# Kernel optimization log

Measured on AMD Instinct MI355X. Metric: run time of the kernel, lower is better.

The kernel has to match this reference:

```python
import jax, jax.numpy as jnp
import numpy as np

N_EMBED = 1024
EMBED_DIM = 64
BETA = 0.25


def setup_inputs() -> dict:
    key = jax.random.key(0)
    k1, k2 = jax.random.split(key)
    # z_e: (B, C, H, W) with C == embed_dim
    z_e = jax.random.normal(k1, (16, EMBED_DIM, 64, 64), dtype=jnp.float32)
    # codebook init: uniform(-1/n_embed, 1/n_embed), matching nn.init.uniform_
    emb = jax.random.uniform(k2, (N_EMBED, EMBED_DIM), dtype=jnp.float32,
                             minval=-1.0 / N_EMBED, maxval=1.0 / N_EMBED)
    return {"z_e": z_e, "emb": emb}


def reference(z_e, emb):
    B, C, H, W = z_e.shape
    # (B,C,H,W) -> (B,H,W,C) -> (B*H*W, C)
    z_flat = jnp.transpose(z_e, (0, 2, 3, 1)).reshape(-1, C)
    # squared euclidean distances to every codebook entry: (N, n_embed)
    dist = (jnp.sum(z_flat * z_flat, axis=1, keepdims=True)
            - 2.0 * (z_flat @ emb.T)
            + jnp.sum(emb * emb, axis=1)[None, :])
    idx = jnp.argmin(dist, axis=1)  # (N,)
    # gather codebook vectors, back to (B, C, H, W)
    z_q = jnp.transpose(emb[idx].reshape(B, H, W, C), (0, 3, 1, 2))
    # straight-through estimator
    z_q_st = z_e + jax.lax.stop_gradient(z_q - z_e)
    codebook_loss = jnp.mean((jax.lax.stop_gradient(z_q) - z_e) ** 2)
    commit_loss = jnp.mean((z_q - jax.lax.stop_gradient(z_e)) ** 2)
    loss = codebook_loss + BETA * commit_loss
    return z_q_st, loss, idx.reshape(B, H, W)
```

## Files before the change

### kernel.cpp

```cpp
#include <hip/hip_runtime.h>

#define NROWS   65536
#define NEMB    1024
#define HWD     4096
#define CHW     262144
#define OUT_ZQ  4194304
#define BETA    0.25f
#define MARGIN  4e-3f
#define MAXC    32

typedef __attribute__((ext_vector_type(8))) short bf16x8;
typedef __attribute__((ext_vector_type(4))) float f32x4;

#define F4C(v,i) ((i)==0?(v).x:((i)==1?(v).y:((i)==2?(v).z:(v).w)))

__device__ __forceinline__ unsigned short bf16rn(float f) {
    unsigned int x = __float_as_uint(f);
    x += 0x7fffu + ((x >> 16) & 1);
    return (unsigned short)(x >> 16);
}
__device__ __forceinline__ float bf16tof(unsigned short h) {
    return __uint_as_float(((unsigned int)h) << 16);
}
__device__ __forceinline__ unsigned int ordf(float f) {
    unsigned int u = __float_as_uint(f);
    return (u & 0x80000000u) ? ~u : (u | 0x80000000u);
}
__device__ __forceinline__ float deordf(unsigned int m) {
    return __uint_as_float((m & 0x80000000u) ? (m ^ 0x80000000u) : ~m);
}

__device__ __forceinline__ float np_pairwise64(const float p[64]) {
#pragma clang fp contract(off)
    float r[8];
#pragma unroll
    for (int a = 0; a < 8; ++a) r[a] = p[a];
#pragma unroll
    for (int i = 8; i < 64; i += 8) {
#pragma unroll
        for (int a = 0; a < 8; ++a) r[a] = r[a] + p[i + a];
    }
    return ((r[0] + r[1]) + (r[2] + r[3])) + ((r[4] + r[5]) + (r[6] + r[7]));
}

__global__ void k_se(const float* __restrict__ emb, float* __restrict__ se) {
#pragma clang fp contract(off)
    int j = blockIdx.x * 256 + threadIdx.x;
    if (j < NEMB) {
        float p[64];
#pragma unroll
        for (int c = 0; c < 64; ++c) { float v = emb[(size_t)j * 64 + c]; p[c] = v * v; }
        se[j] = np_pairwise64(p);
    }
}

__global__ void k_prep(const float* __restrict__ emb, bf16x8* __restrict__ ebt) {
    int idx  = blockIdx.x * 256 + threadIdx.x;
    int tile = idx >> 7;
    int f    = (idx >> 6) & 1;
    int lane = idx & 63;
    int entry = tile * 16 + (lane & 15);
    int kb    = f * 32 + ((lane >> 4) << 3);
    bf16x8 v;
#pragma unroll
    for (int i = 0; i < 8; ++i)
        v[i] = (short)bf16rn(emb[(size_t)entry * 64 + kb + i]);
    ebt[idx] = v;
}

__global__ __launch_bounds__(256, 2) void k_mfma(
        const float* __restrict__ ze, const float* __restrict__ emb,
        const bf16x8* __restrict__ ebt, const float* __restrict__ se,
        float* __restrict__ out, float* __restrict__ wsloss) {
#pragma clang fp contract(off)
    __shared__ float zt[4096];
    __shared__ unsigned short zb[8192];
    __shared__ float se_s[NEMB];
    __shared__ float sz_s[64];
    __shared__ unsigned int rowmin_u[64];
    __shared__ int cnt_s[64];
    __shared__ int cand_s[64 * MAXC];
    __shared__ unsigned long long best_s[64];
    __shared__ int bi_s[64];

    const int tid  = threadIdx.x;
    const int wid  = tid >> 6;
    const int lane = tid & 63;
    const int l15  = lane & 15;
    const int kg   = lane >> 4;
    const int row0 = blockIdx.x * 64;
    const int b    = row0 >> 12;
    const int hw0  = row0 & 4095;
    const float* __restrict__ zblk = ze + (size_t)b * CHW + hw0;

#pragma unroll
    for (int k = 0; k < 4; ++k) se_s[k * 256 + tid] = se[k * 256 + tid];
#pragma unroll
    for (int k = 0; k < 16; ++k) {
        int idx = k * 256 + tid;
        zt[idx] = zblk[(size_t)(idx >> 6) * HWD + (idx & 63)];
    }
    if (tid < 64) { rowmin_u[tid] = 0xFFFFFFFFu; cnt_s[tid] = 0; best_s[tid] = ~0ULL; }
    __syncthreads();

    if (tid < 64) {
        float p[64];
#pragma unroll
        for (int c = 0; c < 64; ++c) { float v = zt[c * 64 + tid]; p[c] = v * v; }
        sz_s[tid] = np_pairwise64(p);
    }

#pragma unroll
    for (int k4 = 0; k4 < 4; ++k4) {
        int cid = k4 * 256 + tid;
        int row = cid >> 4, kc = cid & 15;
        bf16x8 v;
#pragma unroll
        for (int i = 0; i < 8; ++i) {
            int k = kc * 8 + i;
            float z = zt[(k & 63) * 64 + row];
            unsigned short h = bf16rn(z);
            v[i] = (short)((k < 64) ? h : bf16rn(z - bf16tof(h)));
        }
        *(bf16x8*)&zb[(row * 128 + kc * 8) ^ ((row & 7) << 3)] = v;
    }
    __syncthreads();

    const int arow  = wid * 16 + l15;
    const int abase = arow * 128 + kg * 8;
    const int aswz  = (arow & 7) << 3;
    const bf16x8 Ah0 = *(const bf16x8*)&zb[(abase +  0) ^ aswz];
    const bf16x8 Ah1 = *(const bf16x8*)&zb[(abase + 32) ^ aswz];
    const bf16x8 Al0 = *(const bf16x8*)&zb[(abase + 64) ^ aswz];
    const bf16x8 Al1 = *(const bf16x8*)&zb[(abase + 96) ^ aswz];

    float rmin[4] = {3.4028235e38f, 3.4028235e38f, 3.4028235e38f, 3.4028235e38f};
    const bf16x8* __restrict__ ebt_l = ebt + lane;
    const f32x4 zero4 = {0.0f, 0.0f, 0.0f, 0.0f};
    bf16x8 Ca, Cb, Na, Nb;

#define LOADB(T, Xa, Xb) do {                                               \
        const bf16x8* p_ = ebt_l + (T) * 128;                               \
        Xa = p_[0]; Xb = p_[64];                                            \
    } while (0)

#define PROCESS(T, Xa, Xb, PASS2) do {                                      \
        f32x4 acc_ = zero4;                                                 \
        acc_ = __builtin_amdgcn_mfma_f32_16x16x32_bf16(Ah0, Xa, acc_, 0,0,0);\
        acc_ = __builtin_amdgcn_mfma_f32_16x16x32_bf16(Ah1, Xb, acc_, 0,0,0);\
        acc_ = __builtin_amdgcn_mfma_f32_16x16x32_bf16(Al0, Xa, acc_, 0,0,0);\
        acc_ = __builtin_amdgcn_mfma_f32_16x16x32_bf16(Al1, Xb, acc_, 0,0,0);\
        const int j_ = (T) * 16 + l15;                                      \
        const float sej_ = se_s[j_];                                        \
        _Pragma("unroll")                                                   \
        for (int q = 0; q < 4; ++q) {                                       \
            float g_ = fmaf(-2.0f, F4C(acc_, q), sej_);                     \
            if (!(PASS2)) {                                                 \
                rmin[q] = fminf(rmin[q], g_);                               \
            } else if (g_ <= rmin[q]) {                                     \
                int row_ = wid * 16 + kg * 4 + q;                           \
                int k_ = atomicAdd(&cnt_s[row_], 1);                        \
                if (k_ < MAXC) cand_s[row_ * MAXC + k_] = j_;               \
            }                                                               \
        }                                                                   \
    } while (0)

    LOADB(0, Ca, Cb);
    for (int t = 0; t < 64; t += 2) {
        LOADB(t + 1, Na, Nb);
        PROCESS(t, Ca, Cb, false);
        LOADB((t + 2 > 63 ? 63 : t + 2), Ca, Cb);
        PROCESS(t + 1, Na, Nb, false);
    }
#pragma unroll
    for (int q = 0; q < 4; ++q)
        atomicMin(&rowmin_u[wid * 16 + kg * 4 + q], ordf(rmin[q]));
    __syncthreads();
#pragma unroll
    for (int q = 0; q < 4; ++q)
        rmin[q] = deordf(rowmin_u[wid * 16 + kg * 4 + q]) + MARGIN;

    LOADB(0, Ca, Cb);
    for (int t = 0; t < 64; t += 2) {
        LOADB(t + 1, Na, Nb);
        PROCESS(t, Ca, Cb, true);
        LOADB((t + 2 > 63 ? 63 : t + 2), Ca, Cb);
        PROCESS(t + 1, Na, Nb, true);
    }
    __syncthreads();

    for (int w = tid; w < 64 * MAXC; w += 256) {
        int r = w >> 5, ci = w & (MAXC - 1);
        int nc = cnt_s[r];
        if (ci < (nc < MAXC ? nc : MAXC)) {
            int j = cand_s[r * MAXC + ci];
            const float* __restrict__ e = emb + (size_t)j * 64;
            float dot = 0.0f;
#pragma unroll
            for (int c = 0; c < 64; ++c) dot = fmaf(e[c], zt[c * 64 + r], dot);
            float d = (sz_s[r] - 2.0f * dot) + se_s[j];
            atomicMin(&best_s[r],
                      ((unsigned long long)ordf(d) << 32) | (unsigned int)j);
        }
        if (nc > MAXC) {
            for (int j = ci; j < NEMB; j += MAXC) {
                const float* __restrict__ e = emb + (size_t)j * 64;
                float dot = 0.0f;
#pragma unroll
                for (int c = 0; c < 64; ++c) dot = fmaf(e[c], zt[c * 64 + r], dot);
                float d = (sz_s[r] - 2.0f * dot) + se_s[j];
                atomicMin(&best_s[r],
                          ((unsigned long long)ordf(d) << 32) | (unsigned int)j);
            }
        }
    }
    __syncthreads();

    if (tid < 64) {
        int j = (int)(best_s[tid] & 0xFFFFFFFFu);
        bi_s[tid] = j;
        out[(size_t)OUT_ZQ + 1 + row0 + tid] = (float)j;
    }
    __syncthreads();

    float part = 0.0f;
#pragma unroll
    for (int rep = 0; rep < 16; ++rep) {
        int i = rep * 256 + tid;
        int c = i >> 6, r = i & 63;
        int bj = bi_s[r];
        size_t zoff = (size_t)b * CHW + (size_t)c * HWD + hw0 + r;
        float ev = emb[(size_t)bj * 64 + c];
        float zv = ze[zoff];
        float qmz = ev - zv;
        out[zoff] = zv + qmz;
        part = part + qmz * qmz;
    }
    float* red_s = (float*)zb;
    red_s[tid] = part;
    __syncthreads();
#pragma unroll
    for (int s = 128; s >= 1; s >>= 1) {
        if (tid < s) red_s[tid] = red_s[tid] + red_s[tid + s];
        __syncthreads();
    }
    if (tid == 0) wsloss[blockIdx.x] = red_s[0];
#undef LOADB
#undef PROCESS
}

__global__ __launch_bounds__(256, 4) void k_main_v5(
        const float* __restrict__ ze, const float* __restrict__ emb,
        const float* __restrict__ se, float* __restrict__ out,
        float* __restrict__ wsloss) {
#pragma clang fp contract(off)
    __shared__ float zt[4096];
    __shared__ float es[4096];
    __shared__ float se_s[NEMB];
    __shared__ float sz_s[64];
    __shared__ int   bi_s[64];

    const int tid  = threadIdx.x;
    const int rg   = tid & 15;
    const int eg   = tid >> 4;
    const int row0 = blockIdx.x * 64;
    const int b    = row0 >> 12;
    const int hw0  = row0 & 4095;
    const float* __restrict__ zblk = ze + (size_t)b * CHW + hw0;

#pragma unroll
    for (int k = 0; k < 4; ++k) se_s[k * 256 + tid] = se[k * 256 + tid];
#pragma unroll
    for (int k = 0; k < 16; ++k) {
        int idx = k * 256 + tid;
        zt[idx] = zblk[(size_t)(idx >> 6) * HWD + (idx & 63)];
    }
    __syncthreads();
    if (tid < 64) {
        float p[64];
#pragma unroll
        for (int c = 0; c < 64; ++c) { float v = zt[c * 64 + tid]; p[c] = v * v; }
        sz_s[tid] = np_pairwise64(p);
    }
    __syncthreads();
    const float4 sz4 = *(const float4*)&sz_s[rg * 4];
    float best[4] = {3.4028235e38f, 3.4028235e38f, 3.4028235e38f, 3.4028235e38f};
    int   bi[4]   = {0, 0, 0, 0};
    for (int ch = 0; ch < 16; ++ch) {
        __syncthreads();
        {
            const float4* __restrict__ src = (const float4*)(emb + ch * 4096);
#pragma unroll
            for (int k = 0; k < 4; ++k) {
                int idx = k * 256 + tid;
                int jl = idx >> 4, c4 = idx & 15;
                *(float4*)&es[(jl << 6) + ((c4 ^ (jl & 15)) << 2)] = src[idx];
            }
        }
        __syncthreads();
        const float4 se4 = *(const float4*)&se_s[ch * 64 + eg * 4];
        float acc[4][4];
#pragma unroll
        for (int a = 0; a < 4; ++a)
#pragma unroll
            for (int q = 0; q < 4; ++q) acc[a][q] = 0.0f;
#pragma unroll 4
        for (int c4 = 0; c4 < 16; ++c4) {
            float4 zq[4], ef[4];
#pragma unroll
            for (int cc = 0; cc < 4; ++cc)
                zq[cc] = *(const float4*)&zt[((c4 * 4 + cc) << 6) + (rg << 2)];
#pragma unroll
            for (int jj = 0; jj < 4; ++jj) {
                int jl = eg * 4 + jj;
                ef[jj] = *(const float4*)&es[(jl << 6) + ((c4 ^ (jl & 15)) << 2)];
            }
#pragma unroll
            for (int cc = 0; cc < 4; ++cc)
#pragma unroll
                for (int jj = 0; jj < 4; ++jj)
#pragma unroll
                    for (int rr = 0; rr < 4; ++rr)
                        acc[jj][rr] = fmaf(F4C(ef[jj], cc), F4C(zq[cc], rr), acc[jj][rr]);
        }
        const int j0 = ch * 64 + eg * 4;
#pragma unroll
        for (int jj = 0; jj < 4; ++jj) {
            float sej = F4C(se4, jj);
#pragma unroll
            for (int rr = 0; rr < 4; ++rr) {
                float dist = (F4C(sz4, rr) - 2.0f * acc[jj][rr]) + sej;
                if (dist < best[rr]) { best[rr] = dist; bi[rr] = j0 + jj; }
            }
        }
    }
    __syncthreads();
    float* dmin_s = zt;
    int*   imin_s = (int*)es;
#pragma unroll
    for (int rr = 0; rr < 4; ++rr) {
        dmin_s[tid * 4 + rr] = best[rr];
        imin_s[tid * 4 + rr] = bi[rr];
    }
    __syncthreads();
    if (tid < 64) {
        int rgm = tid >> 2, rrm = tid & 3;
        float bb = 3.4028235e38f; int ii = 0x7fffffff;
#pragma unroll
        for (int m = 0; m < 16; ++m) {
            int t = m * 16 + rgm;
            float d  = dmin_s[t * 4 + rrm];
            int   i2 = imin_s[t * 4 + rrm];
            if (d < bb || (d == bb && i2 < ii)) { bb = d; ii = i2; }
        }
        bi_s[tid] = ii;
        out[(size_t)OUT_ZQ + 1 + row0 + tid] = (float)ii;
    }
    __syncthreads();
    float part = 0.0f;
#pragma unroll
    for (int rep = 0; rep < 16; ++rep) {
        int i = rep * 256 + tid;
        int c = i >> 6, r = i & 63;
        int bj = bi_s[r];
        size_t zoff = (size_t)b * CHW + (size_t)c * HWD + hw0 + r;
        float ev = emb[(size_t)bj * 64 + c];
        float zv = ze[zoff];
        float qmz = ev - zv;
        out[zoff] = zv + qmz;
        part = part + qmz * qmz;
    }
    float* red_s = zt;
    red_s[tid] = part;
    __syncthreads();
#pragma unroll
    for (int s = 128; s >= 1; s >>= 1) {
        if (tid < s) red_s[tid] = red_s[tid] + red_s[tid + s];
        __syncthreads();
    }
    if (tid == 0) wsloss[blockIdx.x] = red_s[0];
}

__global__ void k_loss(const float* __restrict__ wsloss, float* __restrict__ out) {
#pragma clang fp contract(off)
    __shared__ float red[256];
    int tid = threadIdx.x;
    float s = 0.0f;
    for (int i = tid; i < 1024; i += 256) s = s + wsloss[i];
    red[tid] = s;
    __syncthreads();
#pragma unroll
    for (int k = 128; k >= 1; k >>= 1) {
        if (tid < k) red[tid] = red[tid] + red[tid + k];
        __syncthreads();
    }
    if (tid == 0) {
        float mse = red[0] / 4194304.0f;
        out[OUT_ZQ] = mse + BETA * mse;
    }
}

extern "C" void kernel_launch(void* const* d_in, const int* in_sizes, int n_in,
                              void* d_out, int out_size, void* d_ws, size_t ws_size,
                              hipStream_t stream) {
    const float* ze  = (const float*)d_in[0];
    const float* emb = (const float*)d_in[1];
    float* out    = (float*)d_out;
    float* se     = (float*)d_ws;
    float* wsloss = se + NEMB;
    bf16x8* ebt   = (bf16x8*)(wsloss + 1024);
    const size_t NEED = 2048 * sizeof(float) + 8192 * sizeof(bf16x8);

    k_se<<<4, 256, 0, stream>>>(emb, se);
    if (ws_size >= NEED) {
        k_prep<<<32,   256, 0, stream>>>(emb, ebt);
        k_mfma<<<1024, 256, 0, stream>>>(ze, emb, ebt, se, out, wsloss);
    } else {
        k_main_v5<<<1024, 256, 0, stream>>>(ze, emb, se, out, wsloss);
    }
    k_loss<<<1, 256, 0, stream>>>(wsloss, out);
}
```

Baseline: 111.0 us.

## Fuse codebook-norm kernel into prep, build MFMA A fragments in registers, shrink MAXC

The separate codebook squared-norm kernel is folded into k_prep, which removes one launch. The split hi/lo bf16 A-operand fragments are now built directly in registers from the transposed z tile instead of going through a swizzled LDS buffer. That drops about 16KB of shared memory and one barrier, and the loss reduction reuses zt as scratch. The per-row candidate cap is halved to 16, which shrinks the candidate list, but any row with more candidates than that falls back to a full 1024-entry scan, so overflow becomes more likely. On the fallback path, k_prep now writes its bf16 table into d_ws, which may overflow the small workspace and clobber se.

```diff
diff --git a/kernel.cpp b/kernel.cpp
--- a/kernel.cpp
+++ b/kernel.cpp
@@ -7,7 +7,7 @@
 #define OUT_ZQ  4194304
 #define BETA    0.25f
 #define MARGIN  4e-3f
-#define MAXC    32
+#define MAXC    16
 
 typedef __attribute__((ext_vector_type(8))) short bf16x8;
 typedef __attribute__((ext_vector_type(4))) float f32x4;
@@ -43,18 +43,9 @@
     return ((r[0] + r[1]) + (r[2] + r[3])) + ((r[4] + r[5]) + (r[6] + r[7]));
 }
 
-__global__ void k_se(const float* __restrict__ emb, float* __restrict__ se) {
+__global__ void k_prep(const float* __restrict__ emb, bf16x8* __restrict__ ebt,
+                       float* __restrict__ se) {
 #pragma clang fp contract(off)
-    int j = blockIdx.x * 256 + threadIdx.x;
-    if (j < NEMB) {
-        float p[64];
-#pragma unroll
-        for (int c = 0; c < 64; ++c) { float v = emb[(size_t)j * 64 + c]; p[c] = v * v; }
-        se[j] = np_pairwise64(p);
-    }
-}
-
-__global__ void k_prep(const float* __restrict__ emb, bf16x8* __restrict__ ebt) {
     int idx  = blockIdx.x * 256 + threadIdx.x;
     int tile = idx >> 7;
     int f    = (idx >> 6) & 1;
@@ -66,6 +57,14 @@
     for (int i = 0; i < 8; ++i)
         v[i] = (short)bf16rn(emb[(size_t)entry * 64 + kb + i]);
     ebt[idx] = v;
+
+    if (blockIdx.x < 4) {
+        int j = blockIdx.x * 256 + threadIdx.x;
+        float p[64];
+#pragma unroll
+        for (int c = 0; c < 64; ++c) { float vv = emb[(size_t)j * 64 + c]; p[c] = vv * vv; }
+        se[j] = np_pairwise64(p);
+    }
 }
 
 __global__ __launch_bounds__(256, 2) void k_mfma(
@@ -74,7 +73,6 @@
         float* __restrict__ out, float* __restrict__ wsloss) {
 #pragma clang fp contract(off)
     __shared__ float zt[4096];
-    __shared__ unsigned short zb[8192];
     __shared__ float se_s[NEMB];
     __shared__ float sz_s[64];
     __shared__ unsigned int rowmin_u[64];
@@ -110,29 +108,20 @@
         sz_s[tid] = np_pairwise64(p);
     }
 
-#pragma unroll
-    for (int k4 = 0; k4 < 4; ++k4) {
-        int cid = k4 * 256 + tid;
-        int row = cid >> 4, kc = cid & 15;
-        bf16x8 v;
-#pragma unroll
-        for (int i = 0; i < 8; ++i) {
-            int k = kc * 8 + i;
-            float z = zt[(k & 63) * 64 + row];
-            unsigned short h = bf16rn(z);
-            v[i] = (short)((k < 64) ? h : bf16rn(z - bf16tof(h)));
-        }
-        *(bf16x8*)&zb[(row * 128 + kc * 8) ^ ((row & 7) << 3)] = v;
-    }
-    __syncthreads();
-
-    const int arow  = wid * 16 + l15;
-    const int abase = arow * 128 + kg * 8;
-    const int aswz  = (arow & 7) << 3;
-    const bf16x8 Ah0 = *(const bf16x8*)&zb[(abase +  0) ^ aswz];
-    const bf16x8 Ah1 = *(const bf16x8*)&zb[(abase + 32) ^ aswz];
-    const bf16x8 Al0 = *(const bf16x8*)&zb[(abase + 64) ^ aswz];
-    const bf16x8 Al1 = *(const bf16x8*)&zb[(abase + 96) ^ aswz];
+    const int arow = wid * 16 + l15;
+    bf16x8 Ah0, Ah1, Al0, Al1;
+#pragma unroll
+    for (int i = 0; i < 8; ++i) {
+        int k0 = kg * 8 + i;
+        float z0 = zt[k0 * 64 + arow];
+        unsigned short h0 = bf16rn(z0);
+        Ah0[i] = (short)h0;
+        Al0[i] = (short)bf16rn(z0 - bf16tof(h0));
+        float z1 = zt[(32 + k0) * 64 + arow];
+        unsigned short h1 = bf16rn(z1);
+        Ah1[i] = (short)h1;
+        Al1[i] = (short)bf16rn(z1 - bf16tof(h1));
+    }
 
     float rmin[4] = {3.4028235e38f, 3.4028235e38f, 3.4028235e38f, 3.4028235e38f};
     const bf16x8* __restrict__ ebt_l = ebt + lane;
@@ -190,7 +179,7 @@
     __syncthreads();
 
     for (int w = tid; w < 64 * MAXC; w += 256) {
-        int r = w >> 5, ci = w & (MAXC - 1);
+        int r = w >> 4, ci = w & (MAXC - 1);
         int nc = cnt_s[r];
         if (ci < (nc < MAXC ? nc : MAXC)) {
             int j = cand_s[r * MAXC + ci];
@@ -236,7 +225,7 @@
         out[zoff] = zv + qmz;
         part = part + qmz * qmz;
     }
-    float* red_s = (float*)zb;
+    float* red_s = zt;
     red_s[tid] = part;
     __syncthreads();
 #pragma unroll
@@ -411,11 +400,11 @@
     bf16x8* ebt   = (bf16x8*)(wsloss + 1024);
     const size_t NEED = 2048 * sizeof(float) + 8192 * sizeof(bf16x8);
 
-    k_se<<<4, 256, 0, stream>>>(emb, se);
     if (ws_size >= NEED) {
-        k_prep<<<32,   256, 0, stream>>>(emb, ebt);
+        k_prep<<<32,   256, 0, stream>>>(emb, ebt, se);
         k_mfma<<<1024, 256, 0, stream>>>(ze, emb, ebt, se, out, wsloss);
     } else {
+        k_prep<<<32, 256, 0, stream>>>(emb, (bf16x8*)d_ws, se);
         k_main_v5<<<1024, 256, 0, stream>>>(ze, emb, se, out, wsloss);
     }
     k_loss<<<1, 256, 0, stream>>>(wsloss, out);
```

After: 158.7 us. 43.0% more time.

## Replace second MFMA pass with per-lane top-2 tracking and fuse codebook norm kernel

Applied to the files above, without the earlier changes.

The candidate search no longer re-runs the MFMA distance pass. Each lane tracks its two smallest approximate distances with their indices, plus a third-smallest value. After the row minimum is reduced, only those two candidates per lane are rescored exactly in fp32. If a lane's third-smallest value also falls within the margin, a flag forces a full fp32 rescan of that row. The hi/lo MFMA accumulations are split into independent chains to shorten dependencies, and the codebook squared-norm kernel is folded into the prep kernel to remove a launch. The cost is extra per-element compare/select work in the main loop and a possible fallback full rescan per flagged row. The fallback path now writes bf16 data into the workspace it may lack room for.

```diff
diff --git a/kernel.cpp b/kernel.cpp
--- a/kernel.cpp
+++ b/kernel.cpp
@@ -7,7 +7,6 @@
 #define OUT_ZQ  4194304
 #define BETA    0.25f
 #define MARGIN  4e-3f
-#define MAXC    32
 
 typedef __attribute__((ext_vector_type(8))) short bf16x8;
 typedef __attribute__((ext_vector_type(4))) float f32x4;
@@ -43,18 +42,9 @@
     return ((r[0] + r[1]) + (r[2] + r[3])) + ((r[4] + r[5]) + (r[6] + r[7]));
 }
 
-__global__ void k_se(const float* __restrict__ emb, float* __restrict__ se) {
+__global__ void k_prep(const float* __restrict__ emb, bf16x8* __restrict__ ebt,
+                       float* __restrict__ se) {
 #pragma clang fp contract(off)
-    int j = blockIdx.x * 256 + threadIdx.x;
-    if (j < NEMB) {
-        float p[64];
-#pragma unroll
-        for (int c = 0; c < 64; ++c) { float v = emb[(size_t)j * 64 + c]; p[c] = v * v; }
-        se[j] = np_pairwise64(p);
-    }
-}
-
-__global__ void k_prep(const float* __restrict__ emb, bf16x8* __restrict__ ebt) {
     int idx  = blockIdx.x * 256 + threadIdx.x;
     int tile = idx >> 7;
     int f    = (idx >> 6) & 1;
@@ -66,6 +56,14 @@
     for (int i = 0; i < 8; ++i)
         v[i] = (short)bf16rn(emb[(size_t)entry * 64 + kb + i]);
     ebt[idx] = v;
+
+    if (blockIdx.x < 4) {
+        int j = blockIdx.x * 256 + threadIdx.x;
+        float p[64];
+#pragma unroll
+        for (int c = 0; c < 64; ++c) { float vv = emb[(size_t)j * 64 + c]; p[c] = vv * vv; }
+        se[j] = np_pairwise64(p);
+    }
 }
 
 __global__ __launch_bounds__(256, 2) void k_mfma(
@@ -78,8 +76,7 @@
     __shared__ float se_s[NEMB];
     __shared__ float sz_s[64];
     __shared__ unsigned int rowmin_u[64];
-    __shared__ int cnt_s[64];
-    __shared__ int cand_s[64 * MAXC];
+    __shared__ int flag_s[64];
     __shared__ unsigned long long best_s[64];
     __shared__ int bi_s[64];
 
@@ -100,7 +97,7 @@
         int idx = k * 256 + tid;
         zt[idx] = zblk[(size_t)(idx >> 6) * HWD + (idx & 63)];
     }
-    if (tid < 64) { rowmin_u[tid] = 0xFFFFFFFFu; cnt_s[tid] = 0; best_s[tid] = ~0ULL; }
+    if (tid < 64) { rowmin_u[tid] = 0xFFFFFFFFu; flag_s[tid] = 0; best_s[tid] = ~0ULL; }
     __syncthreads();
 
     if (tid < 64) {
@@ -134,7 +131,13 @@
     const bf16x8 Al0 = *(const bf16x8*)&zb[(abase + 64) ^ aswz];
     const bf16x8 Al1 = *(const bf16x8*)&zb[(abase + 96) ^ aswz];
 
-    float rmin[4] = {3.4028235e38f, 3.4028235e38f, 3.4028235e38f, 3.4028235e38f};
+    const float INF = 3.4028235e38f;
+    float m1[4] = {INF, INF, INF, INF};
+    float m2[4] = {INF, INF, INF, INF};
+    float m3[4] = {INF, INF, INF, INF};
+    int   a1[4] = {0, 0, 0, 0};
+    int   a2[4] = {0, 0, 0, 0};
+
     const bf16x8* __restrict__ ebt_l = ebt + lane;
     const f32x4 zero4 = {0.0f, 0.0f, 0.0f, 0.0f};
     bf16x8 Ca, Cb, Na, Nb;
@@ -144,66 +147,67 @@
         Xa = p_[0]; Xb = p_[64];                                            \
     } while (0)
 
-#define PROCESS(T, Xa, Xb, PASS2) do {                                      \
-        f32x4 acc_ = zero4;                                                 \
-        acc_ = __builtin_amdgcn_mfma_f32_16x16x32_bf16(Ah0, Xa, acc_, 0,0,0);\
-        acc_ = __builtin_amdgcn_mfma_f32_16x16x32_bf16(Ah1, Xb, acc_, 0,0,0);\
-        acc_ = __builtin_amdgcn_mfma_f32_16x16x32_bf16(Al0, Xa, acc_, 0,0,0);\
-        acc_ = __builtin_amdgcn_mfma_f32_16x16x32_bf16(Al1, Xb, acc_, 0,0,0);\
+#define PROCESS(T, Xa, Xb) do {                                             \
+        f32x4 ah = zero4, al = zero4;                                       \
+        ah = __builtin_amdgcn_mfma_f32_16x16x32_bf16(Ah0, Xa, ah, 0,0,0);   \
+        al = __builtin_amdgcn_mfma_f32_16x16x32_bf16(Al0, Xa, al, 0,0,0);   \
+        ah = __builtin_amdgcn_mfma_f32_16x16x32_bf16(Ah1, Xb, ah, 0,0,0);   \
+        al = __builtin_amdgcn_mfma_f32_16x16x32_bf16(Al1, Xb, al, 0,0,0);   \
         const int j_ = (T) * 16 + l15;                                      \
         const float sej_ = se_s[j_];                                        \
         _Pragma("unroll")                                                   \
         for (int q = 0; q < 4; ++q) {                                       \
-            float g_ = fmaf(-2.0f, F4C(acc_, q), sej_);                     \
-            if (!(PASS2)) {                                                 \
-                rmin[q] = fminf(rmin[q], g_);                               \
-            } else if (g_ <= rmin[q]) {                                     \
-                int row_ = wid * 16 + kg * 4 + q;                           \
-                int k_ = atomicAdd(&cnt_s[row_], 1);                        \
-                if (k_ < MAXC) cand_s[row_ * MAXC + k_] = j_;               \
-            }                                                               \
+            float s_ = F4C(ah, q) + F4C(al, q);                             \
+            float g_ = fmaf(-2.0f, s_, sej_);                               \
+            bool c1 = g_ < m1[q];                                           \
+            bool c2 = g_ < m2[q];                                           \
+            a2[q] = c2 ? (c1 ? a1[q] : j_) : a2[q];                         \
+            a1[q] = c1 ? j_ : a1[q];                                        \
+            float hi1 = fmaxf(m1[q], g_);                                   \
+            m1[q] = fminf(m1[q], g_);                                       \
+            float hi2 = fmaxf(m2[q], hi1);                                  \
+            m2[q] = fminf(m2[q], hi1);                                      \
+            m3[q] = fminf(m3[q], hi2);                                      \
         }                                                                   \
     } while (0)
 
     LOADB(0, Ca, Cb);
     for (int t = 0; t < 64; t += 2) {
         LOADB(t + 1, Na, Nb);
-        PROCESS(t, Ca, Cb, false);
+        PROCESS(t, Ca, Cb);
         LOADB((t + 2 > 63 ? 63 : t + 2), Ca, Cb);
-        PROCESS(t + 1, Na, Nb, false);
+        PROCESS(t + 1, Na, Nb);
     }
 #pragma unroll
     for (int q = 0; q < 4; ++q)
-        atomicMin(&rowmin_u[wid * 16 + kg * 4 + q], ordf(rmin[q]));
-    __syncthreads();
-#pragma unroll
-    for (int q = 0; q < 4; ++q)
-        rmin[q] = deordf(rowmin_u[wid * 16 + kg * 4 + q]) + MARGIN;
-
-    LOADB(0, Ca, Cb);
-    for (int t = 0; t < 64; t += 2) {
-        LOADB(t + 1, Na, Nb);
-        PROCESS(t, Ca, Cb, true);
-        LOADB((t + 2 > 63 ? 63 : t + 2), Ca, Cb);
-        PROCESS(t + 1, Na, Nb, true);
-    }
-    __syncthreads();
-
-    for (int w = tid; w < 64 * MAXC; w += 256) {
-        int r = w >> 5, ci = w & (MAXC - 1);
-        int nc = cnt_s[r];
-        if (ci < (nc < MAXC ? nc : MAXC)) {
-            int j = cand_s[r * MAXC + ci];
-            const float* __restrict__ e = emb + (size_t)j * 64;
-            float dot = 0.0f;
-#pragma unroll
-            for (int c = 0; c < 64; ++c) dot = fmaf(e[c], zt[c * 64 + r], dot);
-            float d = (sz_s[r] - 2.0f * dot) + se_s[j];
-            atomicMin(&best_s[r],
-                      ((unsigned long long)ordf(d) << 32) | (unsigned int)j);
-        }
-        if (nc > MAXC) {
-            for (int j = ci; j < NEMB; j += MAXC) {
+        atomicMin(&rowmin_u[wid * 16 + kg * 4 + q], ordf(m1[q]));
+    __syncthreads();
+
+#pragma unroll
+    for (int q = 0; q < 4; ++q) {
+        const int r = wid * 16 + kg * 4 + q;
+        const float thr = deordf(rowmin_u[r]) + MARGIN;
+        if (m3[q] <= thr) flag_s[r] = 1;
+#pragma unroll
+        for (int s = 0; s < 2; ++s) {
+            float mv = s ? m2[q] : m1[q];
+            int   j  = s ? a2[q] : a1[q];
+            if (mv <= thr) {
+                const float* __restrict__ e = emb + (size_t)j * 64;
+                float dot = 0.0f;
+#pragma unroll
+                for (int c = 0; c < 64; ++c) dot = fmaf(e[c], zt[c * 64 + r], dot);
+                float d = (sz_s[r] - 2.0f * dot) + se_s[j];
+                atomicMin(&best_s[r],
+                          ((unsigned long long)ordf(d) << 32) | (unsigned int)j);
+            }
+        }
+    }
+    __syncthreads();
+
+    for (int r = 0; r < 64; ++r) {
+        if (flag_s[r]) {
+            for (int j = tid; j < NEMB; j += 256) {
                 const float* __restrict__ e = emb + (size_t)j * 64;
                 float dot = 0.0f;
 #pragma unroll
@@ -249,6 +253,7 @@
 #undef PROCESS
 }
 
+#define F4Cv(v,i) F4C(v,i)
 __global__ __launch_bounds__(256, 4) void k_main_v5(
         const float* __restrict__ ze, const float* __restrict__ emb,
         const float* __restrict__ se, float* __restrict__ out,
@@ -321,15 +326,15 @@
                 for (int jj = 0; jj < 4; ++jj)
 #pragma unroll
                     for (int rr = 0; rr < 4; ++rr)
-                        acc[jj][rr] = fmaf(F4C(ef[jj], cc), F4C(zq[cc], rr), acc[jj][rr]);
+                        acc[jj][rr] = fmaf(F4Cv(ef[jj], cc), F4Cv(zq[cc], rr), acc[jj][rr]);
         }
         const int j0 = ch * 64 + eg * 4;
 #pragma unroll
         for (int jj = 0; jj < 4; ++jj) {
-            float sej = F4C(se4, jj);
+            float sej = F4Cv(se4, jj);
 #pragma unroll
             for (int rr = 0; rr < 4; ++rr) {
-                float dist = (F4C(sz4, rr) - 2.0f * acc[jj][rr]) + sej;
+                float dist = (F4Cv(sz4, rr) - 2.0f * acc[jj][rr]) + sej;
                 if (dist < best[rr]) { best[rr] = dist; bi[rr] = j0 + jj; }
             }
         }
@@ -411,11 +416,11 @@
     bf16x8* ebt   = (bf16x8*)(wsloss + 1024);
     const size_t NEED = 2048 * sizeof(float) + 8192 * sizeof(bf16x8);
 
-    k_se<<<4, 256, 0, stream>>>(emb, se);
     if (ws_size >= NEED) {
-        k_prep<<<32,   256, 0, stream>>>(emb, ebt);
+        k_prep<<<32,   256, 0, stream>>>(emb, ebt, se);
         k_mfma<<<1024, 256, 0, stream>>>(ze, emb, ebt, se, out, wsloss);
     } else {
+        k_prep<<<32, 256, 0, stream>>>(emb, (bf16x8*)d_ws, se);
         k_main_v5<<<1024, 256, 0, stream>>>(ze, emb, se, out, wsloss);
     }
     k_loss<<<1, 256, 0, stream>>>(wsloss, out);
```

New measurement: 298.0 us. 2.69x slower.
